# Performance work log

Measured on AMD Instinct MI355X. Metric: run time of the kernel, lower is better.

Reference implementation:

```python
import jax, jax.numpy as jnp
import numpy as np


def build_weights(target):
    """Vectorized version of the per-(batch,frame) distance-weight loop.

    target: [B, T, W, W]. For each frame, find the mean (row, col) coordinate
    of the maximal pixels, then weight = W / (dist_to_center + 1).
    """
    W = target.shape[-1]
    m = jnp.max(target, axis=(-2, -1), keepdims=True)
    mask = (target == m).astype(target.dtype)          # [B,T,W,W]
    cnt = jnp.sum(mask, axis=(-2, -1))                 # [B,T]
    idx = jnp.arange(W, dtype=target.dtype)            # [W]
    # mean row index x and mean col index y of argmax pixels
    x = jnp.sum(jnp.sum(mask, axis=-1) * idx, axis=-1) / cnt  # [B,T]
    y = jnp.sum(jnp.sum(mask, axis=-2) * idx, axis=-1) / cnt  # [B,T]
    a = idx[None, None, :, None] - x[:, :, None, None]  # row offsets [B,T,W,1]
    b = idx[None, None, None, :] - y[:, :, None, None]  # col offsets [B,T,1,W]
    dist = jnp.sqrt(a * a + b * b)                      # [B,T,W,W]
    return W / (dist + 1.0)  # reciprocal of (sqrt(dist)+1)/W


def setup_inputs() -> dict:
    key = jax.random.key(0)
    k1, k2 = jax.random.split(key)
    B, T, W = 16, 16, 256
    inp = jax.random.uniform(k1, (B, 1, T, W, W), dtype=jnp.float32)
    tgt = jax.random.uniform(k2, (B, T, W, W), dtype=jnp.float32)
    return {"input": inp, "target": tgt}


def reference(input, target):
    p = jnp.squeeze(input, axis=1)                 # [B,T,W,W]
    w = build_weights(target)
    # torch binary_cross_entropy clamps log terms at -100
    logp = jnp.clip(jnp.log(p), -100.0)
    log1mp = jnp.clip(jnp.log1p(-p), -100.0)
    loss = -jnp.mean(w * (target * logp + (1.0 - target) * log1mp))
    return loss
```

## Files before the change

### kernel.cpp

```cpp
#include <hip/hip_runtime.h>
#include <hip/hip_bf16.h>
#include <string.h>

#define WDIM 256
#define FRAME (WDIM * WDIM)
#define NFRAMES 256
#define NTOT ((long long)NFRAMES * FRAME)
#define BLOCK 1024


__device__ inline unsigned int pack_bf16x2(float a, float b) {
    __hip_bfloat162 h = __float22bfloat162_rn(make_float2(a, b));
    unsigned int u; memcpy(&u, &h, 4); return u;
}

__global__ __launch_bounds__(BLOCK)
void floss_fused(const float* __restrict__ input, const float* __restrict__ target,
                 double* __restrict__ blocksum) {
    __shared__ unsigned int lds_t[FRAME / 2];
    __shared__ float s_wmax[16];
    __shared__ float s_cnt, s_sr, s_sc;
    __shared__ float s_acc[16];

    const int frame = blockIdx.x;
    const int tid = threadIdx.x;
    const int lane = tid & 63, wave = tid >> 6;

    const float4* __restrict__ t4 = (const float4*)(target + (size_t)frame * FRAME);
    const float4* __restrict__ p4 = (const float4*)(input  + (size_t)frame * FRAME);

    if (tid == 0) { s_cnt = 0.0f; s_sr = 0.0f; s_sc = 0.0f; }

    float lmax = -1.0f;
    #pragma unroll
    for (int k = 0; k < 16; ++k) {
        const int i4 = k * 1024 + tid;
        const float4 v = t4[i4];
        lmax = fmaxf(lmax, fmaxf(fmaxf(v.x, v.y), fmaxf(v.z, v.w)));
        *(uint2*)&lds_t[2 * i4] =
            make_uint2(pack_bf16x2(v.x, v.y), pack_bf16x2(v.z, v.w));
    }

    float4 pva[4], pvb[4];
    #pragma unroll
    for (int k = 0; k < 4; ++k) pva[k] = p4[k * 1024 + tid];

    float wmax = lmax;
    #pragma unroll
    for (int off = 32; off > 0; off >>= 1)
        wmax = fmaxf(wmax, __shfl_down(wmax, off));
    if (lane == 0) s_wmax[wave] = wmax;
    __syncthreads();
    float bmax = s_wmax[0];
    #pragma unroll
    for (int w2 = 1; w2 < 16; ++w2) bmax = fmaxf(bmax, s_wmax[w2]);

    if (lmax == bmax) {
        float cnt = 0.0f, sr = 0.0f, sc = 0.0f;
        const float rowb = (float)wave;
        const float colb = (float)(lane * 4);
        for (int k = 0; k < 16; ++k) {
            const float4 v = t4[k * 1024 + tid];
            const float row = rowb + (float)(16 * k);
            const float vv[4] = {v.x, v.y, v.z, v.w};
            #pragma unroll
            for (int j = 0; j < 4; ++j)
                if (vv[j] == bmax) { cnt += 1.0f; sr += row; sc += colb + (float)j; }
        }
        atomicAdd(&s_cnt, cnt);
        atomicAdd(&s_sr, sr);
        atomicAdd(&s_sc, sc);
    }
    __syncthreads();

    const float rc = __builtin_amdgcn_rcpf(s_cnt);
    const float x = s_sr * rc;
    const float y = s_sc * rc;

    const float drb = (float)wave - x;
    float dc2[4];
    #pragma unroll
    for (int j = 0; j < 4; ++j) {
        const float d = (float)(lane * 4 + j) - y;
        dc2[j] = d * d;
    }

    float acc0 = 0.0f, acc1 = 0.0f;
    #pragma unroll
    for (int c = 0; c < 4; ++c) {
        const float4* cur = (c & 1) ? pvb : pva;
        float4* nxt = (c & 1) ? pva : pvb;
        if (c < 3) {
            #pragma unroll
            for (int k2 = 0; k2 < 4; ++k2)
                nxt[k2] = p4[((c + 1) * 4 + k2) * 1024 + tid];
        }
        #pragma unroll
        for (int k2 = 0; k2 < 4; ++k2) {
            const int k = c * 4 + k2;
            const int i4 = k * 1024 + tid;
            const uint2 tw = *(const uint2*)&lds_t[2 * i4];
            const float tt[4] = {
                __uint_as_float(tw.x << 16),
                __uint_as_float(tw.x & 0xffff0000u),
                __uint_as_float(tw.y << 16),
                __uint_as_float(tw.y & 0xffff0000u)
            };
            const float pp[4] = {cur[k2].x, cur[k2].y, cur[k2].z, cur[k2].w};
            const float dr = drb + (float)(16 * k);
            const float dr2 = dr * dr;
            #pragma unroll
            for (int j = 0; j < 4; ++j) {
                const float dist = __builtin_amdgcn_sqrtf(dr2 + dc2[j]);
                const float w = 256.0f * __builtin_amdgcn_rcpf(dist + 1.0f);
                const float p = pp[j];
                const float lp  = fmaxf(__logf(p), -100.0f);
                const float l1p = fmaxf(__logf(1.0f - p), -100.0f);
                if (j & 1) acc1 += w * fmaf(tt[j], lp - l1p, l1p);
                else       acc0 += w * fmaf(tt[j], lp - l1p, l1p);
            }
        }
    }
    float local = acc0 + acc1;
    #pragma unroll
    for (int off = 32; off > 0; off >>= 1) local += __shfl_down(local, off);
    if (lane == 0) s_acc[wave] = local;
    __syncthreads();
    if (tid == 0) {
        float s = 0.0f;
        #pragma unroll
        for (int w2 = 0; w2 < 16; ++w2) s += s_acc[w2];
        blocksum[frame] = (double)s;
    }
}

__global__ __launch_bounds__(256)
void floss_final(const double* __restrict__ blocksum, float* __restrict__ out) {
    const int tid = threadIdx.x;
    const int lane = tid & 63, wave = tid >> 6;
    double v = blocksum[tid];
    #pragma unroll
    for (int off = 32; off > 0; off >>= 1) v += __shfl_down(v, off);
    __shared__ double sd[4];
    if (lane == 0) sd[wave] = v;
    __syncthreads();
    if (tid == 0)
        out[0] = (float)(-(sd[0] + sd[1] + sd[2] + sd[3]) / (double)NTOT);
}

extern "C" void kernel_launch(void* const* d_in, const int* in_sizes, int n_in,
                              void* d_out, int out_size, void* d_ws, size_t ws_size,
                              hipStream_t stream) {
    const float* input  = (const float*)d_in[0];
    const float* target = (const float*)d_in[1];
    float* out = (float*)d_out;
    double* blocksum = (double*)d_ws;

    floss_fused<<<NFRAMES, BLOCK, 0, stream>>>(input, target, blocksum);
    floss_final<<<1, 256, 0, stream>>>(blocksum, out);
}
```

Measured before the change: 147.8 us.

## Compute BCE terms during target load pass and stash them in LDS and registers

Moves the log-based BCE computation into the first pass, where both target and input are read together with double-buffered loads. The per-element BCE values are kept half in LDS (128KB of float4) and half in registers (32 floats per thread), instead of storing bf16 targets and re-reading input after the max reduction. The goal is to overlap the transcendental work with global loads and to keep the weighted-sum pass short. It raises register pressure and uses the full 128KB of LDS per block. It also drops the bf16 rounding of targets, so the target values used in the loss are exact.

```diff
diff --git a/kernel.cpp b/kernel.cpp
--- a/kernel.cpp
+++ b/kernel.cpp
@@ -1,5 +1,4 @@
 #include <hip/hip_runtime.h>
-#include <hip/hip_bf16.h>
 #include <string.h>
 
 #define WDIM 256
@@ -9,15 +8,10 @@
 #define BLOCK 1024
 
 
-__device__ inline unsigned int pack_bf16x2(float a, float b) {
-    __hip_bfloat162 h = __float22bfloat162_rn(make_float2(a, b));
-    unsigned int u; memcpy(&u, &h, 4); return u;
-}
-
 __global__ __launch_bounds__(BLOCK)
 void floss_fused(const float* __restrict__ input, const float* __restrict__ target,
                  double* __restrict__ blocksum) {
-    __shared__ unsigned int lds_t[FRAME / 2];
+    __shared__ float4 lds_bce[8 * 1024];
     __shared__ float s_wmax[16];
     __shared__ float s_cnt, s_sr, s_sc;
     __shared__ float s_acc[16];
@@ -31,19 +25,44 @@
 
     if (tid == 0) { s_cnt = 0.0f; s_sr = 0.0f; s_sc = 0.0f; }
 
+    float rb[32];
     float lmax = -1.0f;
+
+    float4 tA = t4[tid], pA = p4[tid];
+    float4 tB, pB;
+
     #pragma unroll
     for (int k = 0; k < 16; ++k) {
-        const int i4 = k * 1024 + tid;
-        const float4 v = t4[i4];
-        lmax = fmaxf(lmax, fmaxf(fmaxf(v.x, v.y), fmaxf(v.z, v.w)));
-        *(uint2*)&lds_t[2 * i4] =
-            make_uint2(pack_bf16x2(v.x, v.y), pack_bf16x2(v.z, v.w));
+        float4 tv, pv;
+        if ((k & 1) == 0) { tv = tA; pv = pA; }
+        else              { tv = tB; pv = pB; }
+        if (k < 15) {
+            const int i4 = (k + 1) * 1024 + tid;
+            if ((k & 1) == 0) { tB = t4[i4]; pB = p4[i4]; }
+            else              { tA = t4[i4]; pA = p4[i4]; }
+        }
+
+        lmax = fmaxf(lmax, fmaxf(fmaxf(tv.x, tv.y), fmaxf(tv.z, tv.w)));
+
+        const float tt[4] = {tv.x, tv.y, tv.z, tv.w};
+        const float pp[4] = {pv.x, pv.y, pv.z, pv.w};
+        float b[4];
+        #pragma unroll
+        for (int j = 0; j < 4; ++j) {
+            const float p = pp[j];
+            const float lp  = fmaxf(__logf(p), -100.0f);
+            const float l1p = fmaxf(__logf(1.0f - p), -100.0f);
+            b[j] = fmaf(tt[j], lp - l1p, l1p);
+        }
+        if (k < 8) {
+            lds_bce[k * 1024 + tid] = make_float4(b[0], b[1], b[2], b[3]);
+        } else {
+            rb[(k - 8) * 4 + 0] = b[0];
+            rb[(k - 8) * 4 + 1] = b[1];
+            rb[(k - 8) * 4 + 2] = b[2];
+            rb[(k - 8) * 4 + 3] = b[3];
+        }
     }
-
-    float4 pva[4], pvb[4];
-    #pragma unroll
-    for (int k = 0; k < 4; ++k) pva[k] = p4[k * 1024 + tid];
 
     float wmax = lmax;
     #pragma unroll
@@ -87,38 +106,25 @@
 
     float acc0 = 0.0f, acc1 = 0.0f;
     #pragma unroll
-    for (int c = 0; c < 4; ++c) {
-        const float4* cur = (c & 1) ? pvb : pva;
-        float4* nxt = (c & 1) ? pva : pvb;
-        if (c < 3) {
-            #pragma unroll
-            for (int k2 = 0; k2 < 4; ++k2)
-                nxt[k2] = p4[((c + 1) * 4 + k2) * 1024 + tid];
+    for (int k = 0; k < 16; ++k) {
+        float b[4];
+        if (k < 8) {
+            const float4 v = lds_bce[k * 1024 + tid];
+            b[0] = v.x; b[1] = v.y; b[2] = v.z; b[3] = v.w;
+        } else {
+            b[0] = rb[(k - 8) * 4 + 0];
+            b[1] = rb[(k - 8) * 4 + 1];
+            b[2] = rb[(k - 8) * 4 + 2];
+            b[3] = rb[(k - 8) * 4 + 3];
         }
+        const float dr = drb + (float)(16 * k);
+        const float dr2 = dr * dr;
         #pragma unroll
-        for (int k2 = 0; k2 < 4; ++k2) {
-            const int k = c * 4 + k2;
-            const int i4 = k * 1024 + tid;
-            const uint2 tw = *(const uint2*)&lds_t[2 * i4];
-            const float tt[4] = {
-                __uint_as_float(tw.x << 16),
-                __uint_as_float(tw.x & 0xffff0000u),
-                __uint_as_float(tw.y << 16),
-                __uint_as_float(tw.y & 0xffff0000u)
-            };
-            const float pp[4] = {cur[k2].x, cur[k2].y, cur[k2].z, cur[k2].w};
-            const float dr = drb + (float)(16 * k);
-            const float dr2 = dr * dr;
-            #pragma unroll
-            for (int j = 0; j < 4; ++j) {
-                const float dist = __builtin_amdgcn_sqrtf(dr2 + dc2[j]);
-                const float w = 256.0f * __builtin_amdgcn_rcpf(dist + 1.0f);
-                const float p = pp[j];
-                const float lp  = fmaxf(__logf(p), -100.0f);
-                const float l1p = fmaxf(__logf(1.0f - p), -100.0f);
-                if (j & 1) acc1 += w * fmaf(tt[j], lp - l1p, l1p);
-                else       acc0 += w * fmaf(tt[j], lp - l1p, l1p);
-            }
+        for (int j = 0; j < 4; ++j) {
+            const float dist = __builtin_amdgcn_sqrtf(dr2 + dc2[j]);
+            const float w = 256.0f * __builtin_amdgcn_rcpf(dist + 1.0f);
+            if (j & 1) acc1 += w * b[j];
+            else       acc0 += w * b[j];
         }
     }
     float local = acc0 + acc1;
```

After: 156.8 us. +6.1%, slower.

## Split per-frame fused kernel into stats and BCE kernels over sub-frame blocks

Applied to the files above, without the earlier changes.

Replaces the one-block-per-frame fused kernel (1024 threads, large LDS target copy in bf16) with two kernels over 2048 blocks of 256 threads, each covering one eighth of a frame. The first computes per-subblock max and argmax stats, and the second combines the eight stats per frame and computes the weighted BCE reading target in full precision. This raises parallelism and occupancy and drops the LDS staging, at the cost of reading target twice and an extra launch.

```diff
diff --git a/kernel.cpp b/kernel.cpp
--- a/kernel.cpp
+++ b/kernel.cpp
@@ -1,151 +1,151 @@
 #include <hip/hip_runtime.h>
-#include <hip/hip_bf16.h>
-#include <string.h>
 
 #define WDIM 256
 #define FRAME (WDIM * WDIM)
 #define NFRAMES 256
 #define NTOT ((long long)NFRAMES * FRAME)
-#define BLOCK 1024
+#define NBLK 2048
+#define SUBV4 2048
 
 
-__device__ inline unsigned int pack_bf16x2(float a, float b) {
-    __hip_bfloat162 h = __float22bfloat162_rn(make_float2(a, b));
-    unsigned int u; memcpy(&u, &h, 4); return u;
-}
-
-__global__ __launch_bounds__(BLOCK)
-void floss_fused(const float* __restrict__ input, const float* __restrict__ target,
-                 double* __restrict__ blocksum) {
-    __shared__ unsigned int lds_t[FRAME / 2];
-    __shared__ float s_wmax[16];
-    __shared__ float s_cnt, s_sr, s_sc;
-    __shared__ float s_acc[16];
-
-    const int frame = blockIdx.x;
+__global__ __launch_bounds__(256)
+void floss_stats(const float* __restrict__ target, float4* __restrict__ blk) {
+    const int bid = blockIdx.x;
+    const int fid = bid >> 3, sub = bid & 7;
     const int tid = threadIdx.x;
     const int lane = tid & 63, wave = tid >> 6;
 
-    const float4* __restrict__ t4 = (const float4*)(target + (size_t)frame * FRAME);
-    const float4* __restrict__ p4 = (const float4*)(input  + (size_t)frame * FRAME);
+    const float4* __restrict__ t4 =
+        (const float4*)(target + (size_t)fid * FRAME) + sub * SUBV4;
 
-    if (tid == 0) { s_cnt = 0.0f; s_sr = 0.0f; s_sc = 0.0f; }
+    float4 tv[8];
+    #pragma unroll
+    for (int k = 0; k < 8; ++k) tv[k] = t4[k * 256 + tid];
 
     float lmax = -1.0f;
     #pragma unroll
-    for (int k = 0; k < 16; ++k) {
-        const int i4 = k * 1024 + tid;
-        const float4 v = t4[i4];
-        lmax = fmaxf(lmax, fmaxf(fmaxf(v.x, v.y), fmaxf(v.z, v.w)));
-        *(uint2*)&lds_t[2 * i4] =
-            make_uint2(pack_bf16x2(v.x, v.y), pack_bf16x2(v.z, v.w));
+    for (int k = 0; k < 8; ++k)
+        lmax = fmaxf(lmax, fmaxf(fmaxf(tv[k].x, tv[k].y), fmaxf(tv[k].z, tv[k].w)));
+
+    float wm = lmax;
+    #pragma unroll
+    for (int off = 32; off > 0; off >>= 1) wm = fmaxf(wm, __shfl_down(wm, off));
+    __shared__ float s_wm[4];
+    __shared__ float s_st[4][3];
+    if (lane == 0) s_wm[wave] = wm;
+    __syncthreads();
+    const float bmax = fmaxf(fmaxf(s_wm[0], s_wm[1]), fmaxf(s_wm[2], s_wm[3]));
+
+    float cnt = 0.0f, sr = 0.0f, sc = 0.0f;
+    const float rowb = (float)(sub * 32 + (tid >> 6));
+    const float colb = (float)((tid & 63) * 4);
+    #pragma unroll
+    for (int k = 0; k < 8; ++k) {
+        const float row = rowb + (float)(4 * k);
+        const float vv[4] = {tv[k].x, tv[k].y, tv[k].z, tv[k].w};
+        #pragma unroll
+        for (int j = 0; j < 4; ++j)
+            if (vv[j] == bmax) { cnt += 1.0f; sr += row; sc += colb + (float)j; }
     }
+    #pragma unroll
+    for (int off = 32; off > 0; off >>= 1) {
+        cnt += __shfl_down(cnt, off);
+        sr  += __shfl_down(sr,  off);
+        sc  += __shfl_down(sc,  off);
+    }
+    if (lane == 0) { s_st[wave][0] = cnt; s_st[wave][1] = sr; s_st[wave][2] = sc; }
+    __syncthreads();
+    if (tid == 0) {
+        float c = 0.0f, r = 0.0f, cc = 0.0f;
+        #pragma unroll
+        for (int w = 0; w < 4; ++w) { c += s_st[w][0]; r += s_st[w][1]; cc += s_st[w][2]; }
+        blk[bid] = make_float4(bmax, c, r, cc);
+    }
+}
 
-    float4 pva[4], pvb[4];
+__global__ __launch_bounds__(256)
+void floss_bce(const float* __restrict__ input, const float* __restrict__ target,
+               const float4* __restrict__ blk, double* __restrict__ bsum) {
+    const int bid = blockIdx.x;
+    const int fid = bid >> 3, sub = bid & 7;
+    const int tid = threadIdx.x;
+    const int lane = tid & 63, wave = tid >> 6;
+
+    const float4* __restrict__ t4 =
+        (const float4*)(target + (size_t)fid * FRAME) + sub * SUBV4;
+    const float4* __restrict__ p4 =
+        (const float4*)(input + (size_t)fid * FRAME) + sub * SUBV4;
+
+    float fm = -1.0f;
+    float4 st[8];
     #pragma unroll
-    for (int k = 0; k < 4; ++k) pva[k] = p4[k * 1024 + tid];
+    for (int i = 0; i < 8; ++i) {
+        st[i] = blk[(fid << 3) + i];
+        fm = fmaxf(fm, st[i].x);
+    }
+    float cnt = 0.0f, sr = 0.0f, sc = 0.0f;
+    #pragma unroll
+    for (int i = 0; i < 8; ++i)
+        if (st[i].x == fm) { cnt += st[i].y; sr += st[i].z; sc += st[i].w; }
+    const float rc = __builtin_amdgcn_rcpf(cnt);
+    const float x = sr * rc;
+    const float y = sc * rc;
 
-    float wmax = lmax;
-    #pragma unroll
-    for (int off = 32; off > 0; off >>= 1)
-        wmax = fmaxf(wmax, __shfl_down(wmax, off));
-    if (lane == 0) s_wmax[wave] = wmax;
-    __syncthreads();
-    float bmax = s_wmax[0];
-    #pragma unroll
-    for (int w2 = 1; w2 < 16; ++w2) bmax = fmaxf(bmax, s_wmax[w2]);
-
-    if (lmax == bmax) {
-        float cnt = 0.0f, sr = 0.0f, sc = 0.0f;
-        const float rowb = (float)wave;
-        const float colb = (float)(lane * 4);
-        for (int k = 0; k < 16; ++k) {
-            const float4 v = t4[k * 1024 + tid];
-            const float row = rowb + (float)(16 * k);
-            const float vv[4] = {v.x, v.y, v.z, v.w};
-            #pragma unroll
-            for (int j = 0; j < 4; ++j)
-                if (vv[j] == bmax) { cnt += 1.0f; sr += row; sc += colb + (float)j; }
-        }
-        atomicAdd(&s_cnt, cnt);
-        atomicAdd(&s_sr, sr);
-        atomicAdd(&s_sc, sc);
-    }
-    __syncthreads();
-
-    const float rc = __builtin_amdgcn_rcpf(s_cnt);
-    const float x = s_sr * rc;
-    const float y = s_sc * rc;
-
-    const float drb = (float)wave - x;
+    const float rowb = (float)(sub * 32 + (tid >> 6));
     float dc2[4];
     #pragma unroll
     for (int j = 0; j < 4; ++j) {
-        const float d = (float)(lane * 4 + j) - y;
+        const float d = (float)((tid & 63) * 4 + j) - y;
         dc2[j] = d * d;
     }
 
     float acc0 = 0.0f, acc1 = 0.0f;
     #pragma unroll
-    for (int c = 0; c < 4; ++c) {
-        const float4* cur = (c & 1) ? pvb : pva;
-        float4* nxt = (c & 1) ? pva : pvb;
-        if (c < 3) {
-            #pragma unroll
-            for (int k2 = 0; k2 < 4; ++k2)
-                nxt[k2] = p4[((c + 1) * 4 + k2) * 1024 + tid];
-        }
+    for (int k = 0; k < 8; ++k) {
+        const float4 tv = t4[k * 256 + tid];
+        const float4 pv = p4[k * 256 + tid];
+        const float dr = rowb + (float)(4 * k) - x;
+        const float dr2 = dr * dr;
+        const float tt[4] = {tv.x, tv.y, tv.z, tv.w};
+        const float pp[4] = {pv.x, pv.y, pv.z, pv.w};
         #pragma unroll
-        for (int k2 = 0; k2 < 4; ++k2) {
-            const int k = c * 4 + k2;
-            const int i4 = k * 1024 + tid;
-            const uint2 tw = *(const uint2*)&lds_t[2 * i4];
-            const float tt[4] = {
-                __uint_as_float(tw.x << 16),
-                __uint_as_float(tw.x & 0xffff0000u),
-                __uint_as_float(tw.y << 16),
-                __uint_as_float(tw.y & 0xffff0000u)
-            };
-            const float pp[4] = {cur[k2].x, cur[k2].y, cur[k2].z, cur[k2].w};
-            const float dr = drb + (float)(16 * k);
-            const float dr2 = dr * dr;
-            #pragma unroll
-            for (int j = 0; j < 4; ++j) {
-                const float dist = __builtin_amdgcn_sqrtf(dr2 + dc2[j]);
-                const float w = 256.0f * __builtin_amdgcn_rcpf(dist + 1.0f);
-                const float p = pp[j];
-                const float lp  = fmaxf(__logf(p), -100.0f);
-                const float l1p = fmaxf(__logf(1.0f - p), -100.0f);
-                if (j & 1) acc1 += w * fmaf(tt[j], lp - l1p, l1p);
-                else       acc0 += w * fmaf(tt[j], lp - l1p, l1p);
-            }
+        for (int j = 0; j < 4; ++j) {
+            const float dist = __builtin_amdgcn_sqrtf(dr2 + dc2[j]);
+            const float w = 256.0f * __builtin_amdgcn_rcpf(dist + 1.0f);
+            const float p = pp[j];
+            const float lp  = fmaxf(__logf(p), -100.0f);
+            const float l1p = fmaxf(__logf(1.0f - p), -100.0f);
+            if (j & 1) acc1 += w * fmaf(tt[j], lp - l1p, l1p);
+            else       acc0 += w * fmaf(tt[j], lp - l1p, l1p);
         }
     }
+
     float local = acc0 + acc1;
     #pragma unroll
     for (int off = 32; off > 0; off >>= 1) local += __shfl_down(local, off);
+    __shared__ float s_acc[4];
     if (lane == 0) s_acc[wave] = local;
     __syncthreads();
-    if (tid == 0) {
-        float s = 0.0f;
-        #pragma unroll
-        for (int w2 = 0; w2 < 16; ++w2) s += s_acc[w2];
-        blocksum[frame] = (double)s;
-    }
+    if (tid == 0)
+        bsum[bid] = (double)(s_acc[0] + s_acc[1] + s_acc[2] + s_acc[3]);
 }
 
-__global__ __launch_bounds__(256)
-void floss_final(const double* __restrict__ blocksum, float* __restrict__ out) {
+__global__ __launch_bounds__(1024)
+void floss_final(const double* __restrict__ bsum, float* __restrict__ out) {
     const int tid = threadIdx.x;
     const int lane = tid & 63, wave = tid >> 6;
-    double v = blocksum[tid];
+    double v = bsum[tid] + bsum[tid + 1024];
     #pragma unroll
     for (int off = 32; off > 0; off >>= 1) v += __shfl_down(v, off);
-    __shared__ double sd[4];
+    __shared__ double sd[16];
     if (lane == 0) sd[wave] = v;
     __syncthreads();
-    if (tid == 0)
-        out[0] = (float)(-(sd[0] + sd[1] + sd[2] + sd[3]) / (double)NTOT);
+    if (tid == 0) {
+        double s = 0.0;
+        #pragma unroll
+        for (int w = 0; w < 16; ++w) s += sd[w];
+        out[0] = (float)(-s / (double)NTOT);
+    }
 }
 
 extern "C" void kernel_launch(void* const* d_in, const int* in_sizes, int n_in,
@@ -154,8 +154,10 @@
     const float* input  = (const float*)d_in[0];
     const float* target = (const float*)d_in[1];
     float* out = (float*)d_out;
-    double* blocksum = (double*)d_ws;
+    float4* blk  = (float4*)d_ws;
+    double* bsum = (double*)((char*)d_ws + NBLK * sizeof(float4));
 
-    floss_fused<<<NFRAMES, BLOCK, 0, stream>>>(input, target, blocksum);
-    floss_final<<<1, 256, 0, stream>>>(blocksum, out);
+    floss_stats<<<NBLK, 256, 0, stream>>>(target, blk);
+    floss_bce<<<NBLK, 256, 0, stream>>>(input, target, blk, bsum);
+    floss_final<<<1, 1024, 0, stream>>>(bsum, out);
 }
```

Result: no change. 145.5 us (median of 2 runs) (-1.6%).
